# Optimization experiments

Hardware: AMD Instinct MI355X
Metric: run time of the kernel (lower is better)

## Reference

```python
import jax, jax.numpy as jnp
import numpy as np

B, V = 256, 128000

def setup_inputs() -> dict:
    key = jax.random.key(0)
    k0, k1, k2, k3, k4, k5 = jax.random.split(key, 6)
    logits = jax.random.normal(k0, (B, V), dtype=jnp.float32) * 2.0
    temperatures = jax.random.uniform(k1, (B,), dtype=jnp.float32, minval=0.5, maxval=1.5)
    top_ks = jax.random.randint(k2, (B,), 1, 64, dtype=jnp.int32)
    top_ps = jax.random.uniform(k3, (B,), dtype=jnp.float32, minval=0.8, maxval=1.0)
    min_ps = jax.random.uniform(k4, (B,), dtype=jnp.float32, minval=0.0, maxval=0.1)
    uniform_noise = jax.random.uniform(k5, (B,), dtype=jnp.float32)
    return dict(logits=logits, temperatures=temperatures, top_ks=top_ks,
                top_ps=top_ps, min_ps=min_ps, uniform_noise=uniform_noise)

def _renorm(p):
    return p / jnp.sum(p, axis=-1, keepdims=True)

def _top_k_renorm(probs, top_ks):
    # keep the k largest probs per row, renormalize
    sorted_desc = jnp.sort(probs, axis=-1)[:, ::-1]           # [B,V]
    k_idx = jnp.clip(jnp.maximum(top_ks, 1) - 1, 0, probs.shape[-1] - 1)
    kth = jnp.take_along_axis(sorted_desc, k_idx[:, None], axis=-1)  # [B,1]
    return _renorm(jnp.where(probs >= kth, probs, 0.0))

def _top_p_renorm(probs, top_ps):
    # keep the smallest prefix of sorted probs whose mass covers top_p
    sorted_desc = jnp.sort(probs, axis=-1)[:, ::-1]
    csum = jnp.cumsum(sorted_desc, axis=-1)
    keep = (csum - sorted_desc) < top_ps[:, None]             # cumulative mass before token < p
    thresh = jnp.min(jnp.where(keep, sorted_desc, jnp.inf), axis=-1, keepdims=True)
    return _renorm(jnp.where(probs >= thresh, probs, 0.0))

def _min_p_sample(probs, min_ps, u):
    # keep tokens with prob >= min_p * max_prob, renormalize, inverse-CDF sample
    max_p = jnp.max(probs, axis=-1, keepdims=True)
    probs = _renorm(jnp.where(probs >= min_ps[:, None] * max_p, probs, 0.0))
    cdf = jnp.cumsum(probs, axis=-1)
    target = u[:, None] * cdf[:, -1:]
    tokens = jnp.argmax(cdf >= target, axis=-1).astype(jnp.int32)
    return tokens, probs

def reference(logits, temperatures, top_ks, top_ps, min_ps, uniform_noise):
    probs = jax.nn.softmax(logits.astype(jnp.float32) / temperatures[:, None], axis=-1)
    probs = _top_k_renorm(probs, top_ks)
    probs = _top_p_renorm(probs, top_ps)
    tokens, probs = _min_p_sample(probs, min_ps, uniform_noise)
    return tokens, probs
```

## Files before the change

kernel.cpp:

```cpp
#include <hip/hip_runtime.h>
#include <cmath>


constexpr int BB  = 256;
constexpr int VV  = 128000;
constexpr int CAP = 4096;

__global__ __launch_bounds__(1024) void k_rowmax(const float* __restrict__ logits,
                                                 float* __restrict__ rowmax) {
  const int row = blockIdx.x;
  const float4* lp = reinterpret_cast<const float4*>(logits + (size_t)row * VV);
  float m = -INFINITY;
  for (int j = threadIdx.x; j < VV / 4; j += blockDim.x) {
    float4 v = lp[j];
    m = fmaxf(fmaxf(m, fmaxf(v.x, v.y)), fmaxf(v.z, v.w));
  }
  for (int o = 32; o > 0; o >>= 1) m = fmaxf(m, __shfl_xor(m, o, 64));
  __shared__ float wm[16];
  if ((threadIdx.x & 63) == 0) wm[threadIdx.x >> 6] = m;
  __syncthreads();
  if (threadIdx.x == 0) {
    float mm = wm[0];
    const int nw = blockDim.x >> 6;
    for (int i = 1; i < nw; ++i) mm = fmaxf(mm, wm[i]);
    rowmax[row] = mm;
  }
}

__global__ __launch_bounds__(1024) void k_sample(
    const float* __restrict__ logits, const float* __restrict__ temps,
    const int* __restrict__ topks, const float* __restrict__ topps,
    const float* __restrict__ minps, const float* __restrict__ noise,
    const float* __restrict__ rowmax, float* __restrict__ out) {
  const int row = blockIdx.x;
  const float* lrow = logits + (size_t)row * VV;
  float* orow = out + BB + (size_t)row * VV;

  __shared__ float cl[CAP];
  __shared__ int   ci[CAP];
  __shared__ int   s_cnt;
  __shared__ float s_t, s_tl, s_th;

  const float maxl = rowmax[row];
  if (threadIdx.x == 0) {
    s_t  = 5.0f;
    s_tl = maxl - 40.0f;
    s_th = maxl + 1.0f;
  }
  __syncthreads();

  const float4* lp4 = reinterpret_cast<const float4*>(lrow);
  float4* op4 = reinterpret_cast<float4*>(orow);
  const int nvec = VV / 4;
  const float4 z4 = make_float4(0.f, 0.f, 0.f, 0.f);

  int cnt = 0;
  for (int it = 0; it < 16; ++it) {
    if (threadIdx.x == 0) s_cnt = 0;
    __syncthreads();
    const float t = s_t;
    for (int j = threadIdx.x; j < nvec; j += blockDim.x) {
      const float4 v = lp4[j];
      if (it == 0) op4[j] = z4;
      const int base = j << 2;
      if (v.x >= t) { int p = atomicAdd(&s_cnt, 1); if (p < CAP) { cl[p] = v.x; ci[p] = base;     } }
      if (v.y >= t) { int p = atomicAdd(&s_cnt, 1); if (p < CAP) { cl[p] = v.y; ci[p] = base + 1; } }
      if (v.z >= t) { int p = atomicAdd(&s_cnt, 1); if (p < CAP) { cl[p] = v.z; ci[p] = base + 2; } }
      if (v.w >= t) { int p = atomicAdd(&s_cnt, 1); if (p < CAP) { cl[p] = v.w; ci[p] = base + 3; } }
    }
    __syncthreads();
    cnt = s_cnt;
    if (cnt >= 64 && cnt <= CAP) break;
    if (threadIdx.x == 0) {
      if (cnt > CAP) s_tl = t; else s_th = t;
      s_t = 0.5f * (s_tl + s_th);
    }
    __syncthreads();
  }
  if (cnt > CAP) cnt = CAP;
  const int n = cnt;

  int N = 128;
  while (N < n) N <<= 1;
  for (int j = n + threadIdx.x; j < N; j += blockDim.x) { cl[j] = -INFINITY; ci[j] = 0x7fffffff; }
  __syncthreads();
  for (int kk = 2; kk <= N; kk <<= 1) {
    for (int s = kk >> 1; s > 0; s >>= 1) {
      for (int i = threadIdx.x; i < N; i += blockDim.x) {
        const int l = i ^ s;
        if (l > i) {
          const float a = cl[i], b = cl[l];
          const bool dir = ((i & kk) == 0);
          if ((a < b) == dir) {
            cl[i] = b; cl[l] = a;
            const int ta = ci[i]; ci[i] = ci[l]; ci[l] = ta;
          }
        }
      }
      __syncthreads();
    }
  }

  if (threadIdx.x < 64) {
    const int lane = threadIdx.x;
    const int n64 = min(n, 64);
    const float Tv = temps[row];
    const float Mx = maxl / Tv;
    const bool valid = lane < n64;
    const float lv = valid ? cl[lane] : 0.0f;
    const int   iv = valid ? ci[lane] : 0x7fffffff;
    const float p = valid ? expf(lv / Tv - Mx) : 0.0f;

    int k = topks[row];
    k = max(1, min(k, n64));
    const float kth = __shfl(p, k - 1, 64);
    const bool keepA = valid && (p >= kth);
    float S1 = keepA ? p : 0.0f;
    for (int o = 32; o > 0; o >>= 1) S1 += __shfl_xor(S1, o, 64);
    const float q = keepA ? (p / S1) : 0.0f;

    float cs = q;
    for (int o = 1; o < 64; o <<= 1) { const float v = __shfl_up(cs, o, 64); if (lane >= o) cs += v; }
    const float lhs = cs - q;
    const bool keepBp = keepA && (lhs < topps[row]);
    float thr = keepBp ? q : INFINITY;
    for (int o = 32; o > 0; o >>= 1) thr = fminf(thr, __shfl_xor(thr, o, 64));
    const bool keepB = keepA && (q >= thr);
    float S2 = keepB ? q : 0.0f;
    for (int o = 32; o > 0; o >>= 1) S2 += __shfl_xor(S2, o, 64);
    const float r = keepB ? (q / S2) : 0.0f;

    const float r0 = __shfl(r, 0, 64);
    const bool keepC = keepB && (r >= minps[row] * r0);
    float S3 = keepC ? r : 0.0f;
    for (int o = 32; o > 0; o >>= 1) S3 += __shfl_xor(S3, o, 64);
    const float f = keepC ? (r / S3) : 0.0f;

    float cum = 0.0f, tot = 0.0f;
    for (int i2 = 0; i2 < 64; ++i2) {
      const float fi = __shfl(f, i2, 64);
      const int   ii = __shfl(iv, i2, 64);
      tot += fi;
      if (ii <= iv) cum += fi;
    }
    const float target = noise[row] * tot;
    int tok = 0;
    if (target > 0.0f) {
      int cand = (keepC && cum >= target) ? iv : 0x7fffffff;
      for (int o = 32; o > 0; o >>= 1) cand = min(cand, __shfl_xor(cand, o, 64));
      if (cand == 0x7fffffff) {
        int mi = keepC ? iv : -1;
        for (int o = 32; o > 0; o >>= 1) mi = max(mi, __shfl_xor(mi, o, 64));
        cand = (mi < 0) ? 0 : mi;
      }
      tok = cand;
    }

    if (keepC) orow[iv] = f;
    if (lane == 0) out[row] = (float)tok;
  }
}

extern "C" void kernel_launch(void* const* d_in, const int* in_sizes, int n_in,
                              void* d_out, int out_size, void* d_ws, size_t ws_size,
                              hipStream_t stream) {
  const float* logits = (const float*)d_in[0];
  const float* temps  = (const float*)d_in[1];
  const int*   topks  = (const int*)d_in[2];
  const float* topps  = (const float*)d_in[3];
  const float* minps  = (const float*)d_in[4];
  const float* noise  = (const float*)d_in[5];
  float* out    = (float*)d_out;
  float* rowmax = (float*)d_ws;

  k_rowmax<<<BB, 1024, 0, stream>>>(logits, rowmax);
  k_sample<<<BB, 1024, 0, stream>>>(logits, temps, topks, topps, minps, noise, rowmax, out);
}
```

Baseline: 271.9 us.

## Fuse row max into candidate scan and replace bitonic sort with wave top-64 selection

Merges the separate row-max kernel into the sampling kernel, so one pass over the logits computes the max, zeroes the output and collects candidates above a fixed threshold of 6.0. This removes one full read of the logits and a kernel launch. The threshold bisection runs only when that first pass yields fewer than 64 or more than CAP candidates. CAP drops to 512, and the block-wide bitonic sort with many barriers is replaced by a single wave doing 64 rounds of register argmax. The fixed starting threshold is tuned to the input distribution (normal with std 2), and rows that miss the candidate window still need extra passes.

```diff
diff --git a/kernel.cpp b/kernel.cpp
--- a/kernel.cpp
+++ b/kernel.cpp
@@ -2,113 +2,111 @@
 #include <cmath>
 
 
-constexpr int BB  = 256;
-constexpr int VV  = 128000;
-constexpr int CAP = 4096;
+constexpr int BB   = 256;
+constexpr int VV   = 128000;
+constexpr int CAP  = 512;
+constexpr int NVEC = VV / 4;
+constexpr int IPL  = CAP / 64;
 
-__global__ __launch_bounds__(1024) void k_rowmax(const float* __restrict__ logits,
-                                                 float* __restrict__ rowmax) {
-  const int row = blockIdx.x;
-  const float4* lp = reinterpret_cast<const float4*>(logits + (size_t)row * VV);
-  float m = -INFINITY;
-  for (int j = threadIdx.x; j < VV / 4; j += blockDim.x) {
-    float4 v = lp[j];
-    m = fmaxf(fmaxf(m, fmaxf(v.x, v.y)), fmaxf(v.z, v.w));
-  }
-  for (int o = 32; o > 0; o >>= 1) m = fmaxf(m, __shfl_xor(m, o, 64));
-  __shared__ float wm[16];
-  if ((threadIdx.x & 63) == 0) wm[threadIdx.x >> 6] = m;
-  __syncthreads();
-  if (threadIdx.x == 0) {
-    float mm = wm[0];
-    const int nw = blockDim.x >> 6;
-    for (int i = 1; i < nw; ++i) mm = fmaxf(mm, wm[i]);
-    rowmax[row] = mm;
-  }
-}
-
-__global__ __launch_bounds__(1024) void k_sample(
+__global__ __launch_bounds__(1024) void k_fused(
     const float* __restrict__ logits, const float* __restrict__ temps,
     const int* __restrict__ topks, const float* __restrict__ topps,
     const float* __restrict__ minps, const float* __restrict__ noise,
-    const float* __restrict__ rowmax, float* __restrict__ out) {
+    float* __restrict__ out) {
   const int row = blockIdx.x;
+  const int tid = threadIdx.x;
   const float* lrow = logits + (size_t)row * VV;
   float* orow = out + BB + (size_t)row * VV;
 
   __shared__ float cl[CAP];
   __shared__ int   ci[CAP];
   __shared__ int   s_cnt;
-  __shared__ float s_t, s_tl, s_th;
+  __shared__ float s_t, s_lo, s_hi, s_max;
+  __shared__ float wmax[16];
 
-  const float maxl = rowmax[row];
-  if (threadIdx.x == 0) {
-    s_t  = 5.0f;
-    s_tl = maxl - 40.0f;
-    s_th = maxl + 1.0f;
-  }
+  if (tid == 0) s_cnt = 0;
   __syncthreads();
 
   const float4* lp4 = reinterpret_cast<const float4*>(lrow);
   float4* op4 = reinterpret_cast<float4*>(orow);
-  const int nvec = VV / 4;
   const float4 z4 = make_float4(0.f, 0.f, 0.f, 0.f);
+  const float T0 = 6.0f;
 
-  int cnt = 0;
-  for (int it = 0; it < 16; ++it) {
-    if (threadIdx.x == 0) s_cnt = 0;
+  float m = -INFINITY;
+  for (int j = tid; j < NVEC; j += 1024) {
+    const float4 v = lp4[j];
+    op4[j] = z4;
+    m = fmaxf(fmaxf(fmaxf(v.x, v.y), fmaxf(v.z, v.w)), m);
+    const int base = j << 2;
+    if (v.x >= T0) { int p = atomicAdd(&s_cnt, 1); if (p < CAP) { cl[p] = v.x; ci[p] = base;     } }
+    if (v.y >= T0) { int p = atomicAdd(&s_cnt, 1); if (p < CAP) { cl[p] = v.y; ci[p] = base + 1; } }
+    if (v.z >= T0) { int p = atomicAdd(&s_cnt, 1); if (p < CAP) { cl[p] = v.z; ci[p] = base + 2; } }
+    if (v.w >= T0) { int p = atomicAdd(&s_cnt, 1); if (p < CAP) { cl[p] = v.w; ci[p] = base + 3; } }
+  }
+  for (int o = 32; o > 0; o >>= 1) m = fmaxf(m, __shfl_xor(m, o, 64));
+  if ((tid & 63) == 0) wmax[tid >> 6] = m;
+  __syncthreads();
+  if (tid == 0) {
+    float mm = wmax[0];
+    for (int i = 1; i < 16; ++i) mm = fmaxf(mm, wmax[i]);
+    s_max = mm;
+    s_lo = mm - 40.0f;
+    s_hi = mm + 1.0f;
+  }
+  __syncthreads();
+  int cnt = s_cnt;
+
+  float tcur = T0;
+  for (int it = 0; it < 24 && (cnt < 64 || cnt > CAP); ++it) {
+    if (tid == 0) {
+      if (cnt > CAP) s_lo = tcur; else s_hi = tcur;
+      s_t = 0.5f * (s_lo + s_hi);
+      s_cnt = 0;
+    }
     __syncthreads();
-    const float t = s_t;
-    for (int j = threadIdx.x; j < nvec; j += blockDim.x) {
+    tcur = s_t;
+    for (int j = tid; j < NVEC; j += 1024) {
       const float4 v = lp4[j];
-      if (it == 0) op4[j] = z4;
       const int base = j << 2;
-      if (v.x >= t) { int p = atomicAdd(&s_cnt, 1); if (p < CAP) { cl[p] = v.x; ci[p] = base;     } }
-      if (v.y >= t) { int p = atomicAdd(&s_cnt, 1); if (p < CAP) { cl[p] = v.y; ci[p] = base + 1; } }
-      if (v.z >= t) { int p = atomicAdd(&s_cnt, 1); if (p < CAP) { cl[p] = v.z; ci[p] = base + 2; } }
-      if (v.w >= t) { int p = atomicAdd(&s_cnt, 1); if (p < CAP) { cl[p] = v.w; ci[p] = base + 3; } }
+      if (v.x >= tcur) { int p = atomicAdd(&s_cnt, 1); if (p < CAP) { cl[p] = v.x; ci[p] = base;     } }
+      if (v.y >= tcur) { int p = atomicAdd(&s_cnt, 1); if (p < CAP) { cl[p] = v.y; ci[p] = base + 1; } }
+      if (v.z >= tcur) { int p = atomicAdd(&s_cnt, 1); if (p < CAP) { cl[p] = v.z; ci[p] = base + 2; } }
+      if (v.w >= tcur) { int p = atomicAdd(&s_cnt, 1); if (p < CAP) { cl[p] = v.w; ci[p] = base + 3; } }
     }
     __syncthreads();
     cnt = s_cnt;
-    if (cnt >= 64 && cnt <= CAP) break;
-    if (threadIdx.x == 0) {
-      if (cnt > CAP) s_tl = t; else s_th = t;
-      s_t = 0.5f * (s_tl + s_th);
+  }
+  const int n = min(cnt, CAP);
+
+  if (tid < 64) {
+    const int lane = tid;
+    float rv[IPL]; int rix[IPL];
+#pragma unroll
+    for (int q = 0; q < IPL; ++q) {
+      const int idx = lane + (q << 6);
+      const bool ok = idx < n;
+      rv[q]  = ok ? cl[idx] : -INFINITY;
+      rix[q] = ok ? ci[idx] : 0x7fffffff;
     }
-    __syncthreads();
-  }
-  if (cnt > CAP) cnt = CAP;
-  const int n = cnt;
+    const int n64 = min(n, 64);
+    float lv = 0.0f; int iv = 0x7fffffff;
+    for (int r = 0; r < n64; ++r) {
+      float bv = rv[0]; int bi = rix[0];
+#pragma unroll
+      for (int q = 1; q < IPL; ++q) if (rv[q] > bv) { bv = rv[q]; bi = rix[q]; }
+      for (int o = 32; o > 0; o >>= 1) {
+        const float ov = __shfl_xor(bv, o, 64);
+        const int   oi = __shfl_xor(bi, o, 64);
+        if (ov > bv || (ov == bv && oi < bi)) { bv = ov; bi = oi; }
+      }
+#pragma unroll
+      for (int q = 0; q < IPL; ++q) if (rix[q] == bi) { rv[q] = -INFINITY; rix[q] = 0x7fffffff; }
+      if (lane == r) { lv = bv; iv = bi; }
+    }
 
-  int N = 128;
-  while (N < n) N <<= 1;
-  for (int j = n + threadIdx.x; j < N; j += blockDim.x) { cl[j] = -INFINITY; ci[j] = 0x7fffffff; }
-  __syncthreads();
-  for (int kk = 2; kk <= N; kk <<= 1) {
-    for (int s = kk >> 1; s > 0; s >>= 1) {
-      for (int i = threadIdx.x; i < N; i += blockDim.x) {
-        const int l = i ^ s;
-        if (l > i) {
-          const float a = cl[i], b = cl[l];
-          const bool dir = ((i & kk) == 0);
-          if ((a < b) == dir) {
-            cl[i] = b; cl[l] = a;
-            const int ta = ci[i]; ci[i] = ci[l]; ci[l] = ta;
-          }
-        }
-      }
-      __syncthreads();
-    }
-  }
-
-  if (threadIdx.x < 64) {
-    const int lane = threadIdx.x;
-    const int n64 = min(n, 64);
     const float Tv = temps[row];
-    const float Mx = maxl / Tv;
+    const float Mx = s_max / Tv;
     const bool valid = lane < n64;
-    const float lv = valid ? cl[lane] : 0.0f;
-    const int   iv = valid ? ci[lane] : 0x7fffffff;
     const float p = valid ? expf(lv / Tv - Mx) : 0.0f;
 
     int k = topks[row];
@@ -128,13 +126,13 @@
     const bool keepB = keepA && (q >= thr);
     float S2 = keepB ? q : 0.0f;
     for (int o = 32; o > 0; o >>= 1) S2 += __shfl_xor(S2, o, 64);
-    const float r = keepB ? (q / S2) : 0.0f;
+    const float r2 = keepB ? (q / S2) : 0.0f;
 
-    const float r0 = __shfl(r, 0, 64);
-    const bool keepC = keepB && (r >= minps[row] * r0);
-    float S3 = keepC ? r : 0.0f;
+    const float r0 = __shfl(r2, 0, 64);
+    const bool keepC = keepB && (r2 >= minps[row] * r0);
+    float S3 = keepC ? r2 : 0.0f;
     for (int o = 32; o > 0; o >>= 1) S3 += __shfl_xor(S3, o, 64);
-    const float f = keepC ? (r / S3) : 0.0f;
+    const float f = keepC ? (r2 / S3) : 0.0f;
 
     float cum = 0.0f, tot = 0.0f;
     for (int i2 = 0; i2 < 64; ++i2) {
@@ -170,9 +168,7 @@
   const float* topps  = (const float*)d_in[3];
   const float* minps  = (const float*)d_in[4];
   const float* noise  = (const float*)d_in[5];
-  float* out    = (float*)d_out;
-  float* rowmax = (float*)d_ws;
+  float* out = (float*)d_out;
 
-  k_rowmax<<<BB, 1024, 0, stream>>>(logits, rowmax);
-  k_sample<<<BB, 1024, 0, stream>>>(logits, temps, topks, topps, minps, noise, rowmax, out);
+  k_fused<<<BB, 1024, 0, stream>>>(logits, temps, topks, topps, minps, noise, out);
 }
```

Result: slower. 282.3 us (+3.8%).
